# Performance work log

Measured on AMD Instinct MI355X. Metric: run time of the kernel, lower is better.

Reference implementation:

```python
import jax, jax.numpy as jnp
import numpy as np

B, S, H, D = 8, 2048, 8, 64  # x: [batch, seq, heads, emb_size]; emb_size is per-head dim here


def setup_inputs() -> dict:
    key = jax.random.key(0)
    ks = jax.random.split(key, 9)
    s = 1.0 / np.sqrt(D)
    return {
        "x": jax.random.normal(ks[0], (B, S, H, D), dtype=jnp.float32),
        "Wq": jax.random.uniform(ks[1], (D, D), jnp.float32, -s, s),
        "bq": jax.random.uniform(ks[2], (D,), jnp.float32, -s, s),
        "Wk": jax.random.uniform(ks[3], (D, D), jnp.float32, -s, s),
        "bk": jax.random.uniform(ks[4], (D,), jnp.float32, -s, s),
        "Wv": jax.random.uniform(ks[5], (D, D), jnp.float32, -s, s),
        "bv": jax.random.uniform(ks[6], (D,), jnp.float32, -s, s),
        "Wo": jax.random.uniform(ks[7], (D, D), jnp.float32, -s, s),
        "bo": jax.random.uniform(ks[8], (D,), jnp.float32, -s, s),
    }


def reference(x, Wq, bq, Wk, bk, Wv, bv, Wo, bo):
    # Linear projections on last dim, then permute(0,2,1,3): [b,s,h,d] -> [b,h,s,d]
    q = jnp.einsum('bshd,ed->bhse', x, Wq) + bq
    k = jnp.einsum('bshd,ed->bhse', x, Wk) + bk
    v = jnp.einsum('bshd,ed->bhse', x, Wv) + bv
    energy = jnp.einsum('bhqd,bhkd->bhqk', q, k)  # full O(S^2) score matrix
    scaling = jnp.asarray(D, jnp.float32) ** 0.5  # emb_size ** (1/2), applied post-matmul
    att = jax.nn.softmax(energy / scaling, axis=-1)
    out = jnp.einsum('bhqk,bhkd->bhqd', att, v)
    out = jnp.transpose(out, (0, 2, 1, 3))  # back to [b,s,h,d]
    return jnp.einsum('bshd,ed->bshe', out, Wo) + bo
```

## Files before the change

### kernel.cpp

```cpp
#include <hip/hip_runtime.h>
#include <hip/hip_bf16.h>

#define Bc 8
#define Sc 2048
#define Hc 8
#define Dc 64

#define SCALE_LOG2E 0.18033688011112042f

typedef __bf16 bf16x8 __attribute__((ext_vector_type(8)));
typedef __bf16 bf16x4 __attribute__((ext_vector_type(4)));
typedef float f32x4 __attribute__((ext_vector_type(4)));

__device__ __forceinline__ f32x4 mfma16(bf16x8 a, bf16x8 b, f32x4 c) {
  return __builtin_amdgcn_mfma_f32_16x16x32_bf16(a, b, c, 0, 0, 0);
}

__device__ __forceinline__ bf16x8 cvt8(const float* __restrict__ p) {
  bf16x8 r;
#pragma unroll
  for (int i = 0; i < 8; ++i) r[i] = (__bf16)p[i];
  return r;
}

__device__ __forceinline__ f32x4 zero4() {
  f32x4 z = {0.f, 0.f, 0.f, 0.f};
  return z;
}

typedef __attribute__((address_space(1))) void as1_void;
typedef __attribute__((address_space(3))) void as3_void;

__device__ __forceinline__ void lds_load16(const void* gsrc, void* ldst) {
  __builtin_amdgcn_global_load_lds((as1_void*)(void*)gsrc, (as3_void*)ldst, 16, 0, 0);
}

__global__ __launch_bounds__(256) void qkv_kernel(
    const float* __restrict__ x,
    const float* __restrict__ Wq, const float* __restrict__ bq,
    const float* __restrict__ Wk, const float* __restrict__ bk,
    const float* __restrict__ Wv, const float* __restrict__ bv,
    __bf16* __restrict__ Qb, __bf16* __restrict__ Kb, __bf16* __restrict__ Vt)
{
  const int tid = threadIdx.x;
  const int wid = tid >> 6;
  const int lane = tid & 63;
  const int lr = lane & 15;
  const int lg = lane >> 4;

  const int bid = blockIdx.x;
  const int st = bid & 7;
  const int h  = (bid >> 3) & 7;
  const int b  = bid >> 6;
  const int bh = b * Hc + h;

  bf16x8 wqf[4][2], wkf[4][2], wvf[4][2];
#pragma unroll
  for (int cb = 0; cb < 4; ++cb)
#pragma unroll
    for (int dc = 0; dc < 2; ++dc) {
      const int off = (cb * 16 + lr) * Dc + dc * 32 + lg * 8;
      wqf[cb][dc] = cvt8(Wq + off);
      wkf[cb][dc] = cvt8(Wk + off);
      wvf[cb][dc] = cvt8(Wv + off);
    }
  float bqv[4], bkv[4], bvv[4][4];
#pragma unroll
  for (int cb = 0; cb < 4; ++cb) {
    bqv[cb] = bq[cb * 16 + lr];
    bkv[cb] = bk[cb * 16 + lr];
  }
#pragma unroll
  for (int eb = 0; eb < 4; ++eb)
#pragma unroll
    for (int rr = 0; rr < 4; ++rr) bvv[eb][rr] = bv[eb * 16 + lg * 4 + rr];

#pragma unroll 1
  for (int it = 0; it < 4; ++it) {
    const int s0 = st * 256 + it * 64 + wid * 16;
    bf16x8 xf[2];
#pragma unroll
    for (int dc = 0; dc < 2; ++dc)
      xf[dc] = cvt8(x + ((size_t)(b * Sc + s0 + lr) * Hc + h) * Dc + dc * 32 + lg * 8);

#pragma unroll
    for (int cb = 0; cb < 4; ++cb) {
      f32x4 aq = zero4(), ak = zero4();
      aq = mfma16(xf[0], wqf[cb][0], aq);
      aq = mfma16(xf[1], wqf[cb][1], aq);
      ak = mfma16(xf[0], wkf[cb][0], ak);
      ak = mfma16(xf[1], wkf[cb][1], ak);
#pragma unroll
      for (int rr = 0; rr < 4; ++rr) {
        const size_t row = (size_t)bh * Sc + s0 + lg * 4 + rr;
        Qb[row * Dc + cb * 16 + lr] = (__bf16)((aq[rr] + bqv[cb]) * SCALE_LOG2E);
        Kb[row * Dc + cb * 16 + lr] = (__bf16)(ak[rr] + bkv[cb]);
      }
    }
#pragma unroll
    for (int eb = 0; eb < 4; ++eb) {
      f32x4 av = zero4();
      av = mfma16(wvf[eb][0], xf[0], av);
      av = mfma16(wvf[eb][1], xf[1], av);
#pragma unroll
      for (int rr = 0; rr < 4; ++rr) {
        const int e = eb * 16 + lg * 4 + rr;
        Vt[((size_t)bh * Dc + e) * Sc + s0 + lr] = (__bf16)(av[rr] + bvv[eb][rr]);
      }
    }
  }
}

__global__ __launch_bounds__(256) void attn_kernel(
    const __bf16* __restrict__ Qb, const __bf16* __restrict__ Kb,
    const __bf16* __restrict__ Vt, const float* __restrict__ Wo,
    const float* __restrict__ bo, float* __restrict__ out)
{
  __shared__ __align__(16) __bf16 kls[2][64 * 64];
  __shared__ __align__(16) __bf16 vls[2][64 * 64];
  __shared__ __align__(16) __bf16 pls[4][2][16 * 72];

  const int tid = threadIdx.x;
  const int wid = tid >> 6;
  const int lane = tid & 63;
  const int lr = lane & 15;
  const int lg = lane >> 4;

  const int bid = blockIdx.x;
  const int bh = bid & 63;
  const int qb = bid >> 6;
  const int b = bh >> 3, h = bh & 7;
  const int q0 = qb * 128 + wid * 32;

  const __bf16* Kbase = Kb + (size_t)bh * Sc * Dc;
  const __bf16* Vbase = Vt + (size_t)bh * Dc * Sc;

  bf16x8 qf[2][2];
#pragma unroll
  for (int sub = 0; sub < 2; ++sub)
#pragma unroll
    for (int dc = 0; dc < 2; ++dc)
      qf[sub][dc] = *(const bf16x8*)(Qb +
          ((size_t)bh * Sc + q0 + sub * 16 + lr) * Dc + dc * 32 + lg * 8);

  f32x4 o[2][4];
#pragma unroll
  for (int sub = 0; sub < 2; ++sub)
#pragma unroll
    for (int db = 0; db < 4; ++db) o[sub][db] = zero4();
  float mrow[2] = {-1e30f, -1e30f}, lrow[2] = {0.f, 0.f};

  {
#pragma unroll
    for (int i = 0; i < 2; ++i) {
      const int s = i * 256 + tid, r = s >> 3, c = s & 7;
      lds_load16(Kbase + (size_t)r * Dc + ((c ^ (r & 7)) * 8),
                 &kls[0][(i * 256 + wid * 64) * 8]);
    }
#pragma unroll
    for (int i = 0; i < 2; ++i) {
      const int s = i * 256 + tid, d = s >> 3, c = s & 7;
      lds_load16(Vbase + (size_t)d * Sc + ((c ^ (d & 7)) * 8),
                 &vls[0][(i * 256 + wid * 64) * 8]);
    }
  }

#pragma unroll 1
  for (int kt = 0; kt < Sc / 64; ++kt) {
    const int cur = kt & 1;
    const int nk0 = ((kt + 1) & 31) * 64;
    __builtin_amdgcn_sched_barrier(0);
#pragma unroll
    for (int i = 0; i < 2; ++i) {
      const int s = i * 256 + tid, r = s >> 3, c = s & 7;
      lds_load16(Kbase + (size_t)(nk0 + r) * Dc + ((c ^ (r & 7)) * 8),
                 &kls[cur ^ 1][(i * 256 + wid * 64) * 8]);
    }
#pragma unroll
    for (int i = 0; i < 2; ++i) {
      const int s = i * 256 + tid, d = s >> 3, c = s & 7;
      lds_load16(Vbase + (size_t)d * Sc + nk0 + ((c ^ (d & 7)) * 8),
                 &vls[cur ^ 1][(i * 256 + wid * 64) * 8]);
    }
    asm volatile("s_waitcnt vmcnt(4)" ::: "memory");
    __builtin_amdgcn_sched_barrier(0);
    __builtin_amdgcn_s_barrier();
    __builtin_amdgcn_sched_barrier(0);

    f32x4 e[2][4];
#pragma unroll
    for (int sub = 0; sub < 2; ++sub)
#pragma unroll
      for (int kk = 0; kk < 4; ++kk) e[sub][kk] = zero4();
    __builtin_amdgcn_s_setprio(1);
#pragma unroll
    for (int kk = 0; kk < 4; ++kk) {
      const int row = kk * 16 + lr;
      bf16x8 kf0 = *(const bf16x8*)(&kls[cur][row * 64 + ((lg ^ (row & 7)) * 8)]);
      bf16x8 kf1 = *(const bf16x8*)(&kls[cur][row * 64 + (((4 + lg) ^ (row & 7)) * 8)]);
#pragma unroll
      for (int sub = 0; sub < 2; ++sub) {
        e[sub][kk] = mfma16(kf0, qf[sub][0], e[sub][kk]);
        e[sub][kk] = mfma16(kf1, qf[sub][1], e[sub][kk]);
      }
    }
    __builtin_amdgcn_s_setprio(0);

    asm volatile("s_waitcnt lgkmcnt(0)" ::: "memory");
    __builtin_amdgcn_sched_barrier(0);

#pragma unroll
    for (int sub = 0; sub < 2; ++sub) {
      float tm = e[sub][0][0];
#pragma unroll
      for (int kk = 0; kk < 4; ++kk)
#pragma unroll
        for (int rr = 0; rr < 4; ++rr) tm = fmaxf(tm, e[sub][kk][rr]);
      tm = fmaxf(tm, __shfl_xor(tm, 16));
      tm = fmaxf(tm, __shfl_xor(tm, 32));
      if (!__all(tm - mrow[sub] <= 8.0f)) {
        const float mn = fmaxf(mrow[sub], tm);
        const float al = __builtin_amdgcn_exp2f(mrow[sub] - mn);
#pragma unroll
        for (int db = 0; db < 4; ++db) {
          o[sub][db][0] *= al; o[sub][db][1] *= al;
          o[sub][db][2] *= al; o[sub][db][3] *= al;
        }
        lrow[sub] *= al;
        mrow[sub] = mn;
      }
      float ps = 0.f;
#pragma unroll
      for (int kk = 0; kk < 4; ++kk) {
        const float p0 = __builtin_amdgcn_exp2f(e[sub][kk][0] - mrow[sub]);
        const float p1 = __builtin_amdgcn_exp2f(e[sub][kk][1] - mrow[sub]);
        const float p2 = __builtin_amdgcn_exp2f(e[sub][kk][2] - mrow[sub]);
        const float p3 = __builtin_amdgcn_exp2f(e[sub][kk][3] - mrow[sub]);
        ps += (p0 + p1) + (p2 + p3);
        bf16x4 pk;
        pk[0] = (__bf16)p0; pk[1] = (__bf16)p1;
        pk[2] = (__bf16)p2; pk[3] = (__bf16)p3;
        *(bf16x4*)(&pls[wid][sub][lr * 72 + kk * 16 + lg * 4]) = pk;
      }
      ps += __shfl_xor(ps, 16);
      ps += __shfl_xor(ps, 32);
      lrow[sub] += ps;
    }
    asm volatile("s_waitcnt lgkmcnt(0)" ::: "memory");
    __builtin_amdgcn_sched_barrier(0);

    bf16x8 pa[2][2];
#pragma unroll
    for (int sub = 0; sub < 2; ++sub)
#pragma unroll
      for (int kc = 0; kc < 2; ++kc)
        pa[sub][kc] = *(const bf16x8*)(&pls[wid][sub][lr * 72 + kc * 32 + lg * 8]);
    __builtin_amdgcn_s_setprio(1);
#pragma unroll
    for (int db = 0; db < 4; ++db) {
      const int row = db * 16 + lr;
      bf16x8 vf0 = *(const bf16x8*)(&vls[cur][row * 64 + ((lg ^ (row & 7)) * 8)]);
      bf16x8 vf1 = *(const bf16x8*)(&vls[cur][row * 64 + (((4 + lg) ^ (row & 7)) * 8)]);
#pragma unroll
      for (int sub = 0; sub < 2; ++sub) {
        o[sub][db] = mfma16(pa[sub][0], vf0, o[sub][db]);
        o[sub][db] = mfma16(pa[sub][1], vf1, o[sub][db]);
      }
    }
    __builtin_amdgcn_s_setprio(0);

    asm volatile("s_waitcnt lgkmcnt(0)" ::: "memory");
    __builtin_amdgcn_sched_barrier(0);
    __builtin_amdgcn_s_barrier();
  }

  bf16x8 wof[4][2];
#pragma unroll
  for (int cb = 0; cb < 4; ++cb)
#pragma unroll
    for (int dc = 0; dc < 2; ++dc)
      wof[cb][dc] = cvt8(Wo + (cb * 16 + lr) * Dc + dc * 32 + lg * 8);
  float bov[4];
#pragma unroll
  for (int cb = 0; cb < 4; ++cb) bov[cb] = bo[cb * 16 + lr];

#pragma unroll
  for (int sub = 0; sub < 2; ++sub) {
    const float linv = __builtin_amdgcn_rcpf(lrow[sub]);
    float lis[4];
#pragma unroll
    for (int rr = 0; rr < 4; ++rr) lis[rr] = __shfl(linv, lg * 4 + rr);
    asm volatile("s_waitcnt lgkmcnt(0)" ::: "memory");
    __builtin_amdgcn_sched_barrier(0);
#pragma unroll
    for (int db = 0; db < 4; ++db)
#pragma unroll
      for (int rr = 0; rr < 4; ++rr)
        pls[wid][sub][(lg * 4 + rr) * 72 + db * 16 + lr] =
            (__bf16)(o[sub][db][rr] * lis[rr]);
    asm volatile("s_waitcnt lgkmcnt(0)" ::: "memory");
    __builtin_amdgcn_sched_barrier(0);
    bf16x8 of0 = *(const bf16x8*)(&pls[wid][sub][lr * 72 + lg * 8]);
    bf16x8 of1 = *(const bf16x8*)(&pls[wid][sub][lr * 72 + 32 + lg * 8]);
#pragma unroll
    for (int cb = 0; cb < 4; ++cb) {
      f32x4 acc = zero4();
      acc = mfma16(of0, wof[cb][0], acc);
      acc = mfma16(of1, wof[cb][1], acc);
#pragma unroll
      for (int rr = 0; rr < 4; ++rr) {
        const int s = q0 + sub * 16 + lg * 4 + rr;
        out[(((size_t)b * Sc + s) * Hc + h) * Dc + cb * 16 + lr] = acc[rr] + bov[cb];
      }
    }
  }
}

extern "C" void kernel_launch(void* const* d_in, const int* in_sizes, int n_in,
                              void* d_out, int out_size, void* d_ws, size_t ws_size,
                              hipStream_t stream) {
  const float* x  = (const float*)d_in[0];
  const float* Wq = (const float*)d_in[1];
  const float* bq = (const float*)d_in[2];
  const float* Wk = (const float*)d_in[3];
  const float* bk = (const float*)d_in[4];
  const float* Wv = (const float*)d_in[5];
  const float* bv = (const float*)d_in[6];
  const float* Wo = (const float*)d_in[7];
  const float* bo = (const float*)d_in[8];
  float* outp = (float*)d_out;

  const size_t elems = (size_t)Bc * Hc * Sc * Dc;
  __bf16* Qw = (__bf16*)d_ws;
  __bf16* Kw = Qw + elems;
  __bf16* Vw = Kw + elems;

  qkv_kernel<<<dim3(Bc * Hc * 8), dim3(256), 0, stream>>>(
      x, Wq, bq, Wk, bk, Wv, bv, Qw, Kw, Vw);
  attn_kernel<<<dim3(Bc * Hc * (Sc / 128)), dim3(256), 0, stream>>>(
      Qw, Kw, Vw, Wo, bo, outp);
}
```

Baseline: 243.3 us.

## Switch attention to 32x32 MFMA with register-resident P via permlane swaps

The attention kernel now uses 32x32x16 bf16 MFMA tiles, one 32-row query tile per wave. The S^T layout lets softmax rows reduce with a single cross-half shuffle. The probability matrix is packed to bf16 and rearranged with v_permlane32_swap so it feeds the PV MFMA directly from registers, which removes the per-wave LDS round trip and its waits. The output projection follows the same register path and writes vectorized float4 stores. Separately, the QKV kernel's grid grows 4x with one tile per block instead of a 4-iteration loop, adding parallelism at the cost of reloading the weights per block.

```diff
diff --git a/kernel.cpp b/kernel.cpp
--- a/kernel.cpp
+++ b/kernel.cpp
@@ -9,11 +9,15 @@
 #define SCALE_LOG2E 0.18033688011112042f
 
 typedef __bf16 bf16x8 __attribute__((ext_vector_type(8)));
-typedef __bf16 bf16x4 __attribute__((ext_vector_type(4)));
 typedef float f32x4 __attribute__((ext_vector_type(4)));
+typedef float f32x16 __attribute__((ext_vector_type(16)));
+typedef int i32x4 __attribute__((ext_vector_type(4)));
 
 __device__ __forceinline__ f32x4 mfma16(bf16x8 a, bf16x8 b, f32x4 c) {
   return __builtin_amdgcn_mfma_f32_16x16x32_bf16(a, b, c, 0, 0, 0);
+}
+__device__ __forceinline__ f32x16 mfma32(bf16x8 a, bf16x8 b, f32x16 c) {
+  return __builtin_amdgcn_mfma_f32_32x32x16_bf16(a, b, c, 0, 0, 0);
 }
 
 __device__ __forceinline__ bf16x8 cvt8(const float* __restrict__ p) {
@@ -26,6 +30,18 @@
 __device__ __forceinline__ f32x4 zero4() {
   f32x4 z = {0.f, 0.f, 0.f, 0.f};
   return z;
+}
+__device__ __forceinline__ f32x16 zero16() {
+  f32x16 z;
+#pragma unroll
+  for (int i = 0; i < 16; ++i) z[i] = 0.f;
+  return z;
+}
+
+__device__ __forceinline__ unsigned pkbf16(float lo, float hi) {
+  unsigned short lu = __builtin_bit_cast(unsigned short, (__bf16)lo);
+  unsigned short hu = __builtin_bit_cast(unsigned short, (__bf16)hi);
+  return (unsigned)lu | ((unsigned)hu << 16);
 }
 
 typedef __attribute__((address_space(1))) void as1_void;
@@ -49,9 +65,9 @@
   const int lg = lane >> 4;
 
   const int bid = blockIdx.x;
-  const int st = bid & 7;
-  const int h  = (bid >> 3) & 7;
-  const int b  = bid >> 6;
+  const int st = bid & 31;
+  const int h  = (bid >> 5) & 7;
+  const int b  = bid >> 8;
   const int bh = b * Hc + h;
 
   bf16x8 wqf[4][2], wkf[4][2], wvf[4][2];
@@ -75,38 +91,35 @@
 #pragma unroll
     for (int rr = 0; rr < 4; ++rr) bvv[eb][rr] = bv[eb * 16 + lg * 4 + rr];
 
-#pragma unroll 1
-  for (int it = 0; it < 4; ++it) {
-    const int s0 = st * 256 + it * 64 + wid * 16;
-    bf16x8 xf[2];
-#pragma unroll
-    for (int dc = 0; dc < 2; ++dc)
-      xf[dc] = cvt8(x + ((size_t)(b * Sc + s0 + lr) * Hc + h) * Dc + dc * 32 + lg * 8);
-
-#pragma unroll
-    for (int cb = 0; cb < 4; ++cb) {
-      f32x4 aq = zero4(), ak = zero4();
-      aq = mfma16(xf[0], wqf[cb][0], aq);
-      aq = mfma16(xf[1], wqf[cb][1], aq);
-      ak = mfma16(xf[0], wkf[cb][0], ak);
-      ak = mfma16(xf[1], wkf[cb][1], ak);
-#pragma unroll
-      for (int rr = 0; rr < 4; ++rr) {
-        const size_t row = (size_t)bh * Sc + s0 + lg * 4 + rr;
-        Qb[row * Dc + cb * 16 + lr] = (__bf16)((aq[rr] + bqv[cb]) * SCALE_LOG2E);
-        Kb[row * Dc + cb * 16 + lr] = (__bf16)(ak[rr] + bkv[cb]);
-      }
-    }
-#pragma unroll
-    for (int eb = 0; eb < 4; ++eb) {
-      f32x4 av = zero4();
-      av = mfma16(wvf[eb][0], xf[0], av);
-      av = mfma16(wvf[eb][1], xf[1], av);
-#pragma unroll
-      for (int rr = 0; rr < 4; ++rr) {
-        const int e = eb * 16 + lg * 4 + rr;
-        Vt[((size_t)bh * Dc + e) * Sc + s0 + lr] = (__bf16)(av[rr] + bvv[eb][rr]);
-      }
+  const int s0 = st * 64 + wid * 16;
+  bf16x8 xf[2];
+#pragma unroll
+  for (int dc = 0; dc < 2; ++dc)
+    xf[dc] = cvt8(x + ((size_t)(b * Sc + s0 + lr) * Hc + h) * Dc + dc * 32 + lg * 8);
+
+#pragma unroll
+  for (int cb = 0; cb < 4; ++cb) {
+    f32x4 aq = zero4(), ak = zero4();
+    aq = mfma16(xf[0], wqf[cb][0], aq);
+    aq = mfma16(xf[1], wqf[cb][1], aq);
+    ak = mfma16(xf[0], wkf[cb][0], ak);
+    ak = mfma16(xf[1], wkf[cb][1], ak);
+#pragma unroll
+    for (int rr = 0; rr < 4; ++rr) {
+      const size_t row = (size_t)bh * Sc + s0 + lg * 4 + rr;
+      Qb[row * Dc + cb * 16 + lr] = (__bf16)((aq[rr] + bqv[cb]) * SCALE_LOG2E);
+      Kb[row * Dc + cb * 16 + lr] = (__bf16)(ak[rr] + bkv[cb]);
+    }
+  }
+#pragma unroll
+  for (int eb = 0; eb < 4; ++eb) {
+    f32x4 av = zero4();
+    av = mfma16(wvf[eb][0], xf[0], av);
+    av = mfma16(wvf[eb][1], xf[1], av);
+#pragma unroll
+    for (int rr = 0; rr < 4; ++rr) {
+      const int e = eb * 16 + lg * 4 + rr;
+      Vt[((size_t)bh * Dc + e) * Sc + s0 + lr] = (__bf16)(av[rr] + bvv[eb][rr]);
     }
   }
 }
@@ -118,13 +131,12 @@
 {
   __shared__ __align__(16) __bf16 kls[2][64 * 64];
   __shared__ __align__(16) __bf16 vls[2][64 * 64];
-  __shared__ __align__(16) __bf16 pls[4][2][16 * 72];
 
   const int tid = threadIdx.x;
   const int wid = tid >> 6;
   const int lane = tid & 63;
-  const int lr = lane & 15;
-  const int lg = lane >> 4;
+  const int l31 = lane & 31;
+  const int hi = lane >> 5;
 
   const int bid = blockIdx.x;
   const int bh = bid & 63;
@@ -135,34 +147,28 @@
   const __bf16* Kbase = Kb + (size_t)bh * Sc * Dc;
   const __bf16* Vbase = Vt + (size_t)bh * Dc * Sc;
 
-  bf16x8 qf[2][2];
-#pragma unroll
-  for (int sub = 0; sub < 2; ++sub)
-#pragma unroll
-    for (int dc = 0; dc < 2; ++dc)
-      qf[sub][dc] = *(const bf16x8*)(Qb +
-          ((size_t)bh * Sc + q0 + sub * 16 + lr) * Dc + dc * 32 + lg * 8);
-
-  f32x4 o[2][4];
-#pragma unroll
-  for (int sub = 0; sub < 2; ++sub)
-#pragma unroll
-    for (int db = 0; db < 4; ++db) o[sub][db] = zero4();
-  float mrow[2] = {-1e30f, -1e30f}, lrow[2] = {0.f, 0.f};
-
-  {
-#pragma unroll
-    for (int i = 0; i < 2; ++i) {
-      const int s = i * 256 + tid, r = s >> 3, c = s & 7;
-      lds_load16(Kbase + (size_t)r * Dc + ((c ^ (r & 7)) * 8),
-                 &kls[0][(i * 256 + wid * 64) * 8]);
-    }
-#pragma unroll
-    for (int i = 0; i < 2; ++i) {
-      const int s = i * 256 + tid, d = s >> 3, c = s & 7;
-      lds_load16(Vbase + (size_t)d * Sc + ((c ^ (d & 7)) * 8),
-                 &vls[0][(i * 256 + wid * 64) * 8]);
-    }
+  bf16x8 qf[4];
+#pragma unroll
+  for (int slot = 0; slot < 4; ++slot)
+    qf[slot] = *(const bf16x8*)(Qb + ((size_t)bh * Sc + q0 + l31) * Dc +
+                                slot * 16 + hi * 8);
+
+  f32x16 ot[2];
+  ot[0] = zero16();
+  ot[1] = zero16();
+  float mrow = -1e30f, lrow = 0.f;
+
+#pragma unroll
+  for (int i = 0; i < 2; ++i) {
+    const int s = i * 256 + tid, r = s >> 3, c = s & 7;
+    lds_load16(Kbase + (size_t)r * Dc + ((c ^ (r & 7)) * 8),
+               &kls[0][(i * 256 + wid * 64) * 8]);
+  }
+#pragma unroll
+  for (int i = 0; i < 2; ++i) {
+    const int s = i * 256 + tid, d = s >> 3, c = s & 7;
+    lds_load16(Vbase + (size_t)d * Sc + ((c ^ (d & 7)) * 8),
+               &vls[0][(i * 256 + wid * 64) * 8]);
   }
 
 #pragma unroll 1
@@ -187,133 +193,132 @@
     __builtin_amdgcn_s_barrier();
     __builtin_amdgcn_sched_barrier(0);
 
-    f32x4 e[2][4];
-#pragma unroll
-    for (int sub = 0; sub < 2; ++sub)
-#pragma unroll
-      for (int kk = 0; kk < 4; ++kk) e[sub][kk] = zero4();
+    f32x16 e[2];
+    e[0] = zero16();
+    e[1] = zero16();
     __builtin_amdgcn_s_setprio(1);
 #pragma unroll
-    for (int kk = 0; kk < 4; ++kk) {
-      const int row = kk * 16 + lr;
-      bf16x8 kf0 = *(const bf16x8*)(&kls[cur][row * 64 + ((lg ^ (row & 7)) * 8)]);
-      bf16x8 kf1 = *(const bf16x8*)(&kls[cur][row * 64 + (((4 + lg) ^ (row & 7)) * 8)]);
-#pragma unroll
-      for (int sub = 0; sub < 2; ++sub) {
-        e[sub][kk] = mfma16(kf0, qf[sub][0], e[sub][kk]);
-        e[sub][kk] = mfma16(kf1, qf[sub][1], e[sub][kk]);
+    for (int kg = 0; kg < 2; ++kg) {
+      const int r = kg * 32 + l31;
+#pragma unroll
+      for (int slot = 0; slot < 4; ++slot) {
+        bf16x8 kf = *(const bf16x8*)(
+            &kls[cur][r * 64 + (((slot * 2 + hi) ^ (r & 7)) * 8)]);
+        e[kg] = mfma32(kf, qf[slot], e[kg]);
       }
     }
     __builtin_amdgcn_s_setprio(0);
 
-    asm volatile("s_waitcnt lgkmcnt(0)" ::: "memory");
-    __builtin_amdgcn_sched_barrier(0);
-
-#pragma unroll
-    for (int sub = 0; sub < 2; ++sub) {
-      float tm = e[sub][0][0];
-#pragma unroll
-      for (int kk = 0; kk < 4; ++kk)
-#pragma unroll
-        for (int rr = 0; rr < 4; ++rr) tm = fmaxf(tm, e[sub][kk][rr]);
-      tm = fmaxf(tm, __shfl_xor(tm, 16));
-      tm = fmaxf(tm, __shfl_xor(tm, 32));
-      if (!__all(tm - mrow[sub] <= 8.0f)) {
-        const float mn = fmaxf(mrow[sub], tm);
-        const float al = __builtin_amdgcn_exp2f(mrow[sub] - mn);
-#pragma unroll
-        for (int db = 0; db < 4; ++db) {
-          o[sub][db][0] *= al; o[sub][db][1] *= al;
-          o[sub][db][2] *= al; o[sub][db][3] *= al;
-        }
-        lrow[sub] *= al;
-        mrow[sub] = mn;
+    float t0[8];
+#pragma unroll
+    for (int i = 0; i < 8; ++i)
+      t0[i] = fmaxf(fmaxf(e[0][i], e[0][i + 8]), fmaxf(e[1][i], e[1][i + 8]));
+    float tm = fmaxf(fmaxf(fmaxf(t0[0], t0[1]), fmaxf(t0[2], t0[3])),
+                     fmaxf(fmaxf(t0[4], t0[5]), fmaxf(t0[6], t0[7])));
+    tm = fmaxf(tm, __shfl_xor(tm, 32));
+    if (!__all(tm - mrow <= 8.0f)) {
+      const float mn = fmaxf(mrow, tm);
+      const float al = __builtin_amdgcn_exp2f(mrow - mn);
+#pragma unroll
+      for (int i = 0; i < 16; ++i) { ot[0][i] *= al; ot[1][i] *= al; }
+      lrow *= al;
+      mrow = mn;
+    }
+#pragma unroll
+    for (int kg = 0; kg < 2; ++kg)
+#pragma unroll
+      for (int i = 0; i < 16; ++i)
+        e[kg][i] = __builtin_amdgcn_exp2f(e[kg][i] - mrow);
+    {
+      float s[4] = {0.f, 0.f, 0.f, 0.f};
+#pragma unroll
+      for (int kg = 0; kg < 2; ++kg)
+#pragma unroll
+        for (int i = 0; i < 16; ++i) s[i & 3] += e[kg][i];
+      float ps = (s[0] + s[1]) + (s[2] + s[3]);
+      ps += __shfl_xor(ps, 32);
+      lrow += ps;
+    }
+
+    unsigned pw[4][4];
+#pragma unroll
+    for (int kg = 0; kg < 2; ++kg)
+#pragma unroll
+      for (int hf = 0; hf < 2; ++hf) {
+        unsigned a0 = pkbf16(e[kg][8 * hf + 0], e[kg][8 * hf + 1]);
+        unsigned a1 = pkbf16(e[kg][8 * hf + 2], e[kg][8 * hf + 3]);
+        unsigned b0 = pkbf16(e[kg][8 * hf + 4], e[kg][8 * hf + 5]);
+        unsigned b1 = pkbf16(e[kg][8 * hf + 6], e[kg][8 * hf + 7]);
+        asm volatile("v_permlane32_swap_b32 %0, %1" : "+v"(a0), "+v"(b0));
+        asm volatile("v_permlane32_swap_b32 %0, %1" : "+v"(a1), "+v"(b1));
+        const int slot = 2 * kg + hf;
+        pw[slot][0] = a0; pw[slot][1] = a1; pw[slot][2] = b0; pw[slot][3] = b1;
       }
-      float ps = 0.f;
-#pragma unroll
-      for (int kk = 0; kk < 4; ++kk) {
-        const float p0 = __builtin_amdgcn_exp2f(e[sub][kk][0] - mrow[sub]);
-        const float p1 = __builtin_amdgcn_exp2f(e[sub][kk][1] - mrow[sub]);
-        const float p2 = __builtin_amdgcn_exp2f(e[sub][kk][2] - mrow[sub]);
-        const float p3 = __builtin_amdgcn_exp2f(e[sub][kk][3] - mrow[sub]);
-        ps += (p0 + p1) + (p2 + p3);
-        bf16x4 pk;
-        pk[0] = (__bf16)p0; pk[1] = (__bf16)p1;
-        pk[2] = (__bf16)p2; pk[3] = (__bf16)p3;
-        *(bf16x4*)(&pls[wid][sub][lr * 72 + kk * 16 + lg * 4]) = pk;
+
+    __builtin_amdgcn_s_setprio(1);
+#pragma unroll
+    for (int dg = 0; dg < 2; ++dg) {
+      const int r = dg * 32 + l31;
+#pragma unroll
+      for (int slot = 0; slot < 4; ++slot) {
+        bf16x8 vf = *(const bf16x8*)(
+            &vls[cur][r * 64 + (((slot * 2 + hi) ^ (r & 7)) * 8)]);
+        i32x4 w = {(int)pw[slot][0], (int)pw[slot][1],
+                   (int)pw[slot][2], (int)pw[slot][3]};
+        ot[dg] = mfma32(vf, __builtin_bit_cast(bf16x8, w), ot[dg]);
       }
-      ps += __shfl_xor(ps, 16);
-      ps += __shfl_xor(ps, 32);
-      lrow[sub] += ps;
-    }
-    asm volatile("s_waitcnt lgkmcnt(0)" ::: "memory");
-    __builtin_amdgcn_sched_barrier(0);
-
-    bf16x8 pa[2][2];
-#pragma unroll
-    for (int sub = 0; sub < 2; ++sub)
-#pragma unroll
-      for (int kc = 0; kc < 2; ++kc)
-        pa[sub][kc] = *(const bf16x8*)(&pls[wid][sub][lr * 72 + kc * 32 + lg * 8]);
-    __builtin_amdgcn_s_setprio(1);
-#pragma unroll
-    for (int db = 0; db < 4; ++db) {
-      const int row = db * 16 + lr;
-      bf16x8 vf0 = *(const bf16x8*)(&vls[cur][row * 64 + ((lg ^ (row & 7)) * 8)]);
-      bf16x8 vf1 = *(const bf16x8*)(&vls[cur][row * 64 + (((4 + lg) ^ (row & 7)) * 8)]);
-#pragma unroll
-      for (int sub = 0; sub < 2; ++sub) {
-        o[sub][db] = mfma16(pa[sub][0], vf0, o[sub][db]);
-        o[sub][db] = mfma16(pa[sub][1], vf1, o[sub][db]);
-      }
     }
     __builtin_amdgcn_s_setprio(0);
 
-    asm volatile("s_waitcnt lgkmcnt(0)" ::: "memory");
-    __builtin_amdgcn_sched_barrier(0);
     __builtin_amdgcn_s_barrier();
   }
 
-  bf16x8 wof[4][2];
-#pragma unroll
-  for (int cb = 0; cb < 4; ++cb)
-#pragma unroll
-    for (int dc = 0; dc < 2; ++dc)
-      wof[cb][dc] = cvt8(Wo + (cb * 16 + lr) * Dc + dc * 32 + lg * 8);
-  float bov[4];
-#pragma unroll
-  for (int cb = 0; cb < 4; ++cb) bov[cb] = bo[cb * 16 + lr];
-
-#pragma unroll
-  for (int sub = 0; sub < 2; ++sub) {
-    const float linv = __builtin_amdgcn_rcpf(lrow[sub]);
-    float lis[4];
-#pragma unroll
-    for (int rr = 0; rr < 4; ++rr) lis[rr] = __shfl(linv, lg * 4 + rr);
-    asm volatile("s_waitcnt lgkmcnt(0)" ::: "memory");
-    __builtin_amdgcn_sched_barrier(0);
-#pragma unroll
-    for (int db = 0; db < 4; ++db)
-#pragma unroll
-      for (int rr = 0; rr < 4; ++rr)
-        pls[wid][sub][(lg * 4 + rr) * 72 + db * 16 + lr] =
-            (__bf16)(o[sub][db][rr] * lis[rr]);
-    asm volatile("s_waitcnt lgkmcnt(0)" ::: "memory");
-    __builtin_amdgcn_sched_barrier(0);
-    bf16x8 of0 = *(const bf16x8*)(&pls[wid][sub][lr * 72 + lg * 8]);
-    bf16x8 of1 = *(const bf16x8*)(&pls[wid][sub][lr * 72 + 32 + lg * 8]);
-#pragma unroll
-    for (int cb = 0; cb < 4; ++cb) {
-      f32x4 acc = zero4();
-      acc = mfma16(of0, wof[cb][0], acc);
-      acc = mfma16(of1, wof[cb][1], acc);
-#pragma unroll
-      for (int rr = 0; rr < 4; ++rr) {
-        const int s = q0 + sub * 16 + lg * 4 + rr;
-        out[(((size_t)b * Sc + s) * Hc + h) * Dc + cb * 16 + lr] = acc[rr] + bov[cb];
-      }
-    }
-  }
+  const float linv = __builtin_amdgcn_rcpf(lrow);
+#pragma unroll
+  for (int dg = 0; dg < 2; ++dg)
+#pragma unroll
+    for (int i = 0; i < 16; ++i) ot[dg][i] *= linv;
+
+  unsigned ow[4][4];
+#pragma unroll
+  for (int dg = 0; dg < 2; ++dg)
+#pragma unroll
+    for (int hf = 0; hf < 2; ++hf) {
+      unsigned a0 = pkbf16(ot[dg][8 * hf + 0], ot[dg][8 * hf + 1]);
+      unsigned a1 = pkbf16(ot[dg][8 * hf + 2], ot[dg][8 * hf + 3]);
+      unsigned b0 = pkbf16(ot[dg][8 * hf + 4], ot[dg][8 * hf + 5]);
+      unsigned b1 = pkbf16(ot[dg][8 * hf + 6], ot[dg][8 * hf + 7]);
+      asm volatile("v_permlane32_swap_b32 %0, %1" : "+v"(a0), "+v"(b0));
+      asm volatile("v_permlane32_swap_b32 %0, %1" : "+v"(a1), "+v"(b1));
+      const int slot = 2 * dg + hf;
+      ow[slot][0] = a0; ow[slot][1] = a1; ow[slot][2] = b0; ow[slot][3] = b1;
+    }
+
+  f32x16 oacc[2];
+  oacc[0] = zero16();
+  oacc[1] = zero16();
+#pragma unroll
+  for (int eg = 0; eg < 2; ++eg) {
+#pragma unroll
+    for (int slot = 0; slot < 4; ++slot) {
+      bf16x8 wf = cvt8(Wo + (eg * 32 + l31) * Dc + slot * 16 + hi * 8);
+      i32x4 w = {(int)ow[slot][0], (int)ow[slot][1],
+                 (int)ow[slot][2], (int)ow[slot][3]};
+      oacc[eg] = mfma32(wf, __builtin_bit_cast(bf16x8, w), oacc[eg]);
+    }
+  }
+
+  const size_t srow = ((size_t)b * Sc + q0 + l31) * Hc + h;
+#pragma unroll
+  for (int eg = 0; eg < 2; ++eg)
+#pragma unroll
+    for (int c = 0; c < 4; ++c) {
+      const f32x4 bo4 = *(const f32x4*)(bo + eg * 32 + c * 8 + hi * 4);
+      f32x4 v;
+#pragma unroll
+      for (int j = 0; j < 4; ++j) v[j] = oacc[eg][4 * c + j] + bo4[j];
+      *(f32x4*)(out + srow * Dc + eg * 32 + c * 8 + hi * 4) = v;
+    }
 }
 
 extern "C" void kernel_launch(void* const* d_in, const int* in_sizes, int n_in,
@@ -335,7 +340,7 @@
   __bf16* Kw = Qw + elems;
   __bf16* Vw = Kw + elems;
 
-  qkv_kernel<<<dim3(Bc * Hc * 8), dim3(256), 0, stream>>>(
+  qkv_kernel<<<dim3(Bc * Hc * 32), dim3(256), 0, stream>>>(
       x, Wq, bq, Wk, bk, Wv, bv, Qw, Kw, Vw);
   attn_kernel<<<dim3(Bc * Hc * (Sc / 128)), dim3(256), 0, stream>>>(
       Qw, Kw, Vw, Wo, bo, outp);
```

Result: slower. 259.7 us (+6.7%).
